# Performance work log

Measured on AMD Instinct MI355X. Metric: run time of the kernel, lower is better.

## Reference

```python
import jax, jax.numpy as jnp
import numpy as np

N, E = 50000, 800000          # nodes, directed edges
IN_DIM, HC, OUT_DIM = 128, 64, 128
NEG_SLOPE = 0.2               # PyG GATConv default leaky_relu slope
EPS = 1e-5                    # PyG LayerNorm default eps


def setup_inputs() -> dict:
    key = jax.random.key(0)
    ks = jax.random.split(key, 10)
    s = 0.1
    return {
        "x": jax.random.normal(ks[0], (N, IN_DIM), jnp.float32),
        "edge_index": jax.random.randint(ks[1], (2, E), 0, N, dtype=jnp.int32),
        # conv1: GATConv(IN_DIM -> HC, heads=2, concat=True)
        "W1": jax.random.normal(ks[2], (IN_DIM, 2 * HC), jnp.float32) * s,
        "att_src1": jax.random.normal(ks[3], (2, HC), jnp.float32) * s,
        "att_dst1": jax.random.normal(ks[4], (2, HC), jnp.float32) * s,
        "b1": jnp.zeros((2 * HC,), jnp.float32),
        "ln1_w": jnp.ones((2 * HC,), jnp.float32),
        "ln1_b": jnp.zeros((2 * HC,), jnp.float32),
        # conv2: GATConv(2*HC -> OUT_DIM, heads=1, concat=False)
        "W2": jax.random.normal(ks[5], (2 * HC, OUT_DIM), jnp.float32) * s,
        "att_src2": jax.random.normal(ks[6], (1, OUT_DIM), jnp.float32) * s,
        "att_dst2": jax.random.normal(ks[7], (1, OUT_DIM), jnp.float32) * s,
        "b2": jnp.zeros((OUT_DIM,), jnp.float32),
        "ln2_w": jnp.ones((OUT_DIM,), jnp.float32),
        "ln2_b": jnp.zeros((OUT_DIM,), jnp.float32),
    }


def gat_conv(x, src, dst, W, att_src, att_dst, bias, heads, C, concat):
    """PyG GATConv (shared lin for src/dst, self-loops already in src/dst)."""
    n = x.shape[0]
    h = (x @ W).reshape(n, heads, C)                       # [N,H,C]
    a_src = jnp.einsum('nhc,hc->nh', h, att_src)           # [N,H]
    a_dst = jnp.einsum('nhc,hc->nh', h, att_dst)           # [N,H]
    e = jax.nn.leaky_relu(a_src[src] + a_dst[dst], NEG_SLOPE)   # [E',H]
    # numerically-stable softmax over incoming edges of each dst node
    emax = jax.ops.segment_max(e, dst, num_segments=n)     # [N,H] (self-loops => non-empty)
    ex = jnp.exp(e - emax[dst])
    denom = jax.ops.segment_sum(ex, dst, num_segments=n)
    alpha = ex / (denom[dst] + 1e-16)                      # [E',H]
    out = jax.ops.segment_sum(h[src] * alpha[:, :, None], dst, num_segments=n)  # [N,H,C]
    out = out.reshape(n, heads * C) if concat else out.mean(axis=1)
    return out + bias


def graph_layernorm(x, w, b):
    """PyG LayerNorm, mode='graph', single graph: normalize over ALL nodes+features."""
    mean = x.mean()
    xc = x - mean
    var = (xc * xc).mean()
    return xc * jax.lax.rsqrt(var + EPS) * w + b


def reference(x, edge_index, W1, att_src1, att_dst1, b1, ln1_w, ln1_b,
              W2, att_src2, att_dst2, b2, ln2_w, ln2_b):
    n = x.shape[0]
    loop = jnp.arange(n, dtype=edge_index.dtype)
    src = jnp.concatenate([edge_index[0], loop])           # add self-loops for GAT convs
    dst = jnp.concatenate([edge_index[1], loop])

    h = gat_conv(x, src, dst, W1, att_src1, att_dst1, b1, heads=2, C=HC, concat=True)
    h = jax.nn.relu(graph_layernorm(h, ln1_w, ln1_b))
    h = gat_conv(h, src, dst, W2, att_src2, att_dst2, b2, heads=1, C=OUT_DIM, concat=False)
    h = graph_layernorm(h, ln2_w, ln2_b)

    # SimpleConv(aggr='mean') over the ORIGINAL edges (no self-loops), then residual
    s0, d0 = edge_index[0], edge_index[1]
    agg = jax.ops.segment_sum(h[s0], d0, num_segments=n)
    cnt = jax.ops.segment_sum(jnp.ones(s0.shape, h.dtype), d0, num_segments=n)
    mean_agg = agg / jnp.maximum(cnt, 1.0)[:, None]
    return jax.nn.relu(mean_agg + x)
```

## Files before the change

### kernel.cpp

```cpp
#include <hip/hip_runtime.h>
#include <hip/hip_bf16.h>
#include <cstdint>
#include <cstddef>

#define NN 50000
#define EE 800000
#define DD 128
#define NEG 0.2f
#define EPSL 1e-5f

#define NB   196
#define EPB  4096
#define NBKT 196
#define HM   (NBKT * NB)

#define GROWS 64

typedef __hip_bfloat16 bf16;
typedef short short8 __attribute__((ext_vector_type(8)));
typedef float f32x4 __attribute__((ext_vector_type(4)));

__device__ inline float bflo(unsigned u) { return __uint_as_float(u << 16); }
__device__ inline float bfhi(unsigned u) { return __uint_as_float(u & 0xffff0000u); }

__device__ inline unsigned short f2bf(float f) {
    __bf16 h = (__bf16)f;
    return __builtin_bit_cast(unsigned short, h);
}
__device__ inline unsigned pack2(float a, float b) {
    return (unsigned)f2bf(a) | ((unsigned)f2bf(b) << 16);
}

__device__ inline void store4(float* Out, size_t idx, float4 v) {
    *(float4*)&Out[idx] = v;
}
__device__ inline void store4(bf16* Out, size_t idx, float4 v) {
    union { bf16 b[4]; ushort4 u; } cv;
    cv.b[0] = (bf16)v.x; cv.b[1] = (bf16)v.y; cv.b[2] = (bf16)v.z; cv.b[3] = (bf16)v.w;
    *(ushort4*)&Out[idx] = cv.u;
}


__global__ __launch_bounds__(256) void hist_kernel(const int* __restrict__ ei,
                                                   int* __restrict__ histG) {
    __shared__ int lh[NBKT];
    int tid = threadIdx.x;
    for (int t = tid; t < NBKT; t += 256) lh[t] = 0;
    __syncthreads();
    int base = blockIdx.x * EPB;
    #pragma unroll
    for (int j = 0; j < EPB / 256; ++j) {
        int i = base + j * 256 + tid;
        if (i < EE) {
            unsigned d = (unsigned)ei[EE + i];
            atomicAdd(&lh[d >> 8], 1);
        }
    }
    __syncthreads();
    for (int t = tid; t < NBKT; t += 256) histG[t * NB + blockIdx.x] = lh[t];
}

__global__ __launch_bounds__(1024) void scan_hist_kernel(const int* __restrict__ histG,
                                                         int* __restrict__ offs,
                                                         int* __restrict__ bstart) {
    __shared__ int wsum[16];
    __shared__ int carry_s;
    int tid = threadIdx.x, lane = tid & 63, wv = tid >> 6;
    if (tid == 0) carry_s = 0;
    __syncthreads();
    for (int base = 0; base < HM; base += 4096) {
        int i4 = base + tid * 4;
        int4 v = make_int4(0, 0, 0, 0);
        if (i4 + 3 < HM) v = *(const int4*)&histG[i4];
        else {
            if (i4 + 0 < HM) v.x = histG[i4 + 0];
            if (i4 + 1 < HM) v.y = histG[i4 + 1];
            if (i4 + 2 < HM) v.z = histG[i4 + 2];
            if (i4 + 3 < HM) v.w = histG[i4 + 3];
        }
        int tsum = v.x + v.y + v.z + v.w;
        int x = tsum;
        for (int off = 1; off < 64; off <<= 1) {
            int t = __shfl_up(x, off);
            if (lane >= off) x += t;
        }
        if (lane == 63) wsum[wv] = x;
        __syncthreads();
        if (wv == 0) {
            int s = (lane < 16) ? wsum[lane] : 0;
            for (int off = 1; off < 16; off <<= 1) {
                int t = __shfl_up(s, off);
                if (lane >= off) s += t;
            }
            if (lane < 16) wsum[lane] = s;
        }
        __syncthreads();
        int waveoff = (wv == 0) ? 0 : wsum[wv - 1];
        int carry = carry_s;
        int o0 = carry + waveoff + x - tsum;
        int o1 = o0 + v.x, o2 = o1 + v.y, o3 = o2 + v.z;
        if (i4 + 3 < HM) *(int4*)&offs[i4] = make_int4(o0, o1, o2, o3);
        else {
            if (i4 + 0 < HM) offs[i4 + 0] = o0;
            if (i4 + 1 < HM) offs[i4 + 1] = o1;
            if (i4 + 2 < HM) offs[i4 + 2] = o2;
            if (i4 + 3 < HM) offs[i4 + 3] = o3;
        }
        if (i4 < HM && (i4 % NB) == 0) bstart[i4 / NB] = o0;
        __syncthreads();
        if (tid == 0) carry_s += wsum[15];
        __syncthreads();
    }
    if (tid == 0) bstart[NBKT] = carry_s;
}

__global__ __launch_bounds__(256) void scatter_pass1_kernel(const int* __restrict__ ei,
                                                            const int* __restrict__ offs,
                                                            unsigned* __restrict__ tmp) {
    __shared__ int lofs[NBKT];
    int tid = threadIdx.x;
    for (int t = tid; t < NBKT; t += 256) lofs[t] = offs[t * NB + blockIdx.x];
    __syncthreads();
    int base = blockIdx.x * EPB;
    #pragma unroll
    for (int j = 0; j < EPB / 256; ++j) {
        int i = base + j * 256 + tid;
        if (i < EE) {
            unsigned s = (unsigned)ei[i];
            unsigned d = (unsigned)ei[EE + i];
            unsigned key = (d << 16) | s;
            int pos = atomicAdd(&lofs[d >> 8], 1);
            tmp[pos] = key;
        }
    }
}

__global__ __launch_bounds__(256) void bucket_sort_kernel(const unsigned* __restrict__ tmp,
                                                          const int* __restrict__ bstart,
                                                          unsigned* __restrict__ col,
                                                          int* __restrict__ row_ptr) {
    __shared__ int cnt[256];
    __shared__ int cpos[256];
    __shared__ int wtot[4];
    int tid = threadIdx.x, lane = tid & 63, wv = tid >> 6;
    int s0 = bstart[blockIdx.x], s1 = bstart[blockIdx.x + 1];
    cnt[tid] = 0;
    __syncthreads();
    for (int i = s0 + tid; i < s1; i += 256)
        atomicAdd(&cnt[(tmp[i] >> 16) & 0xFF], 1);
    __syncthreads();
    int v = cnt[tid];
    int x = v;
    for (int off = 1; off < 64; off <<= 1) {
        int t = __shfl_up(x, off);
        if (lane >= off) x += t;
    }
    if (lane == 63) wtot[wv] = x;
    __syncthreads();
    int add = 0;
    for (int k = 0; k < wv; ++k) add += wtot[k];
    int start = s0 + add + x - v;
    cpos[tid] = start;
    int d = blockIdx.x * 256 + tid;
    if (d <= NN) row_ptr[d] = start;
    __syncthreads();
    for (int i = s0 + tid; i < s1; i += 256) {
        unsigned key = tmp[i];
        int pos = atomicAdd(&cpos[(key >> 16) & 0xFF], 1);
        col[pos] = key;
    }
}

template <int H, bool LN>
__global__ __launch_bounds__(512) void gemm_attn(const float* __restrict__ X,
                                                 const float* __restrict__ W,
                                                 const float* __restrict__ att_s,
                                                 const float* __restrict__ att_d,
                                                 const double* __restrict__ stats,
                                                 const float* __restrict__ lnw,
                                                 const float* __restrict__ lnb,
                                                 bf16* __restrict__ Hout,
                                                 float* __restrict__ a_src,
                                                 float* __restrict__ a_dst) {
    __shared__ __align__(16) char lds[(128 * 136 + 64 * 136) * 2 + 2048];
    unsigned short* Bt = (unsigned short*)lds;
    unsigned short* As = (unsigned short*)(lds + 128 * 136 * 2);
    float* Cs = (float*)lds;
    float* psum = (float*)(lds + (128 * 136 + 64 * 136) * 2);

    int tid = threadIdx.x;
    int row0 = blockIdx.x * GROWS;

    {
        int c = tid & 127, kg = tid >> 7;
        #pragma unroll 2
        for (int i = 0; i < 8; ++i) {
            int k0 = i * 16 + kg * 4;
            float wa = W[(size_t)(k0 + 0) * DD + c];
            float wb = W[(size_t)(k0 + 1) * DD + c];
            float wcv = W[(size_t)(k0 + 2) * DD + c];
            float wdv = W[(size_t)(k0 + 3) * DD + c];
            uint2 pk = make_uint2(pack2(wa, wb), pack2(wcv, wdv));
            *(uint2*)&Bt[c * 136 + k0] = pk;
        }
    }
    {
        int sub = tid & 31, rq = tid >> 5;
        int c4 = sub * 4;
        float mean = 0.f, inv = 1.f;
        float4 lw4 = make_float4(1.f, 1.f, 1.f, 1.f), lb4 = make_float4(0.f, 0.f, 0.f, 0.f);
        if (LN) {
            const double M = (double)NN * DD;
            double mean_d = stats[0] / M;
            double var_d = stats[1] / M - mean_d * mean_d;
            mean = (float)mean_d;
            inv = rsqrtf((float)var_d + EPSL);
            lw4 = *(const float4*)&lnw[c4];
            lb4 = *(const float4*)&lnb[c4];
        }
        #pragma unroll
        for (int i = 0; i < 4; ++i) {
            int r = i * 16 + rq;
            int row = row0 + r;
            float4 xv = make_float4(0.f, 0.f, 0.f, 0.f);
            if (row < NN) xv = *(const float4*)&X[(size_t)row * DD + c4];
            if (LN) {
                xv.x = fmaxf((xv.x - mean) * inv * lw4.x + lb4.x, 0.f);
                xv.y = fmaxf((xv.y - mean) * inv * lw4.y + lb4.y, 0.f);
                xv.z = fmaxf((xv.z - mean) * inv * lw4.z + lb4.z, 0.f);
                xv.w = fmaxf((xv.w - mean) * inv * lw4.w + lb4.w, 0.f);
            }
            uint2 pk = make_uint2(pack2(xv.x, xv.y), pack2(xv.z, xv.w));
            *(uint2*)&As[r * 136 + c4] = pk;
        }
    }
    __syncthreads();

    int lane = tid & 63, w = tid >> 6;
    int rg = w & 3, cg = w >> 2;
    int l15 = lane & 15, quad = lane >> 4;
    f32x4 acc[4];
    #pragma unroll
    for (int t = 0; t < 4; ++t) acc[t] = 0.f;
    const unsigned short* Arow = As + (rg * 16 + l15) * 136 + quad * 8;
    const unsigned short* Brow = Bt + l15 * 136 + quad * 8;
    #pragma unroll
    for (int ks = 0; ks < 4; ++ks) {
        short8 a = *(const short8*)(Arow + ks * 32);
        #pragma unroll
        for (int tt = 0; tt < 4; ++tt) {
            short8 b = *(const short8*)(Brow + (cg * 4 + tt) * 16 * 136 + ks * 32);
            acc[tt] = __builtin_amdgcn_mfma_f32_16x16x32_bf16(a, b, acc[tt], 0, 0, 0);
        }
    }
    __syncthreads();

    #pragma unroll
    for (int tt = 0; tt < 4; ++tt)
        #pragma unroll
        for (int r = 0; r < 4; ++r)
            Cs[(rg * 16 + quad * 4 + r) * 132 + (cg * 4 + tt) * 16 + l15] = acc[tt][r];

    float ds[4] = {0.f, 0.f, 0.f, 0.f}, dd[4] = {0.f, 0.f, 0.f, 0.f};
    #pragma unroll
    for (int tt = 0; tt < 4; ++tt) {
        int cc = (cg * 4 + tt) * 16 + l15;
        float as_ = att_s[cc], ad_ = att_d[cc];
        #pragma unroll
        for (int r = 0; r < 4; ++r) {
            ds[r] = fmaf(acc[tt][r], as_, ds[r]);
            dd[r] = fmaf(acc[tt][r], ad_, dd[r]);
        }
    }
    #pragma unroll
    for (int off = 1; off < 16; off <<= 1) {
        #pragma unroll
        for (int r = 0; r < 4; ++r) {
            ds[r] += __shfl_xor(ds[r], off);
            dd[r] += __shfl_xor(dd[r], off);
        }
    }
    if (l15 == 0) {
        #pragma unroll
        for (int r = 0; r < 4; ++r) {
            int rr = rg * 16 + quad * 4 + r;
            int row = row0 + rr;
            if (H == 2) {
                if (row < NN) {
                    a_src[row * 2 + cg] = ds[r];
                    a_dst[row * 2 + cg] = dd[r];
                }
            } else {
                psum[cg * 64 + rr] = ds[r];
                psum[128 + cg * 64 + rr] = dd[r];
            }
        }
    }
    __syncthreads();

    if (H == 1 && tid < 64) {
        int row = row0 + tid;
        if (row < NN) {
            a_src[row] = psum[tid] + psum[64 + tid];
            a_dst[row] = psum[128 + tid] + psum[192 + tid];
        }
    }

    {
        int sub = tid & 31, rq = tid >> 5;
        int c4 = sub * 4;
        unsigned short* Hp = (unsigned short*)Hout;
        #pragma unroll
        for (int i = 0; i < 4; ++i) {
            int r = i * 16 + rq;
            int row = row0 + r;
            if (row < NN) {
                float4 cv = *(const float4*)&Cs[r * 132 + c4];
                ushort4 pk;
                pk.x = f2bf(cv.x); pk.y = f2bf(cv.y);
                pk.z = f2bf(cv.z); pk.w = f2bf(cv.w);
                *(ushort4*)&Hp[(size_t)row * DD + c4] = pk;
            }
        }
    }
}

template <int H, typename OT>
__global__ __launch_bounds__(256) void gat_agg(const int* __restrict__ row_ptr,
                                               const unsigned* __restrict__ col,
                                               const bf16* __restrict__ Hin,
                                               const float* __restrict__ a_src,
                                               const float* __restrict__ a_dst,
                                               const float* __restrict__ bias,
                                               OT* __restrict__ Out,
                                               float2* __restrict__ pstats) {
    int tid = threadIdx.x;
    int sl = tid & 31;
    int n = blockIdx.x * 8 + (tid >> 5);
    int c0 = sl * 4;
    const int head4 = (H == 2) ? (sl >> 4) : 0;

    int beg = row_ptr[n], end = row_ptr[n + 1];
    int deg = end - beg;

    float ad0 = a_dst[n * H + 0];
    float ad1 = (H == 2) ? a_dst[n * H + 1] : 0.f;
    const ushort* Hp = (const ushort*)Hin + c0;

    float acc[4] = {0.f, 0.f, 0.f, 0.f};
    float dl0 = 0.f, dl1 = 0.f;

    for (int base = 0; base < deg; base += 32) {
        int ecnt = min(32, deg - base);
        int sv = 0; float w0v = 0.f, w1v = 0.f;
        if (sl < ecnt) {
            sv = (int)(col[beg + base + sl] & 0xffffu);
            if (H == 2) {
                float2 av = *(const float2*)&a_src[sv * 2];
                float e0 = av.x + ad0; e0 = (e0 > 0.f) ? e0 : NEG * e0;
                float e1 = av.y + ad1; e1 = (e1 > 0.f) ? e1 : NEG * e1;
                w0v = __expf(e0); w1v = __expf(e1);
                dl0 += w0v; dl1 += w1v;
            } else {
                float e0 = a_src[sv] + ad0; e0 = (e0 > 0.f) ? e0 : NEG * e0;
                w0v = __expf(e0);
                dl0 += w0v;
            }
        }
        int j = 0;
        for (; j + 7 < ecnt; j += 8) {
            int s[8]; float ww[8];
            uint2 h[8];
            #pragma unroll
            for (int u = 0; u < 8; ++u) {
                s[u] = __shfl(sv, j + u, 32);
                if (H == 2) {
                    float a0 = __shfl(w0v, j + u, 32), b0 = __shfl(w1v, j + u, 32);
                    ww[u] = head4 ? b0 : a0;
                } else {
                    ww[u] = __shfl(w0v, j + u, 32);
                }
            }
            #pragma unroll
            for (int u = 0; u < 8; ++u) h[u] = *(const uint2*)(Hp + (size_t)s[u] * DD);
            #pragma unroll
            for (int u = 0; u < 8; ++u) {
                acc[0] = fmaf(ww[u], bflo(h[u].x), acc[0]);
                acc[1] = fmaf(ww[u], bfhi(h[u].x), acc[1]);
                acc[2] = fmaf(ww[u], bflo(h[u].y), acc[2]);
                acc[3] = fmaf(ww[u], bfhi(h[u].y), acc[3]);
            }
        }
        for (; j < ecnt; ++j) {
            int s = __shfl(sv, j, 32);
            float w;
            if (H == 2) {
                float a0 = __shfl(w0v, j, 32), b0 = __shfl(w1v, j, 32);
                w = head4 ? b0 : a0;
            } else {
                w = __shfl(w0v, j, 32);
            }
            uint2 hv = *(const uint2*)(Hp + (size_t)s * DD);
            acc[0] = fmaf(w, bflo(hv.x), acc[0]); acc[1] = fmaf(w, bfhi(hv.x), acc[1]);
            acc[2] = fmaf(w, bflo(hv.y), acc[2]); acc[3] = fmaf(w, bfhi(hv.y), acc[3]);
        }
    }

    #pragma unroll
    for (int off = 1; off < 32; off <<= 1) {
        dl0 += __shfl_xor(dl0, off);
        if (H == 2) dl1 += __shfl_xor(dl1, off);
    }

    float e0 = a_src[n * H + 0] + ad0; e0 = (e0 > 0.f) ? e0 : NEG * e0;
    float ws0 = __expf(e0);
    float ws1 = 0.f;
    if (H == 2) {
        float e1 = a_src[n * H + 1] + ad1; e1 = (e1 > 0.f) ? e1 : NEG * e1;
        ws1 = __expf(e1);
    }
    float den = (H == 2 && head4) ? (dl1 + ws1) : (dl0 + ws0);
    float wself = (H == 2 && head4) ? ws1 : ws0;
    float rinv = 1.f / (den + 1e-16f);
    uint2 hs = *(const uint2*)(Hp + (size_t)n * DD);
    float4 bi = *(const float4*)&bias[c0];
    float4 o;
    o.x = fmaf(wself, bflo(hs.x), acc[0]) * rinv + bi.x;
    o.y = fmaf(wself, bfhi(hs.x), acc[1]) * rinv + bi.y;
    o.z = fmaf(wself, bflo(hs.y), acc[2]) * rinv + bi.z;
    o.w = fmaf(wself, bfhi(hs.y), acc[3]) * rinv + bi.w;
    store4(Out, (size_t)n * DD + c0, o);

    float t1 = o.x + o.y + o.z + o.w;
    float t2 = o.x * o.x + o.y * o.y + o.z * o.z + o.w * o.w;
    #pragma unroll
    for (int off = 1; off < 32; off <<= 1) {
        t1 += __shfl_xor(t1, off);
        t2 += __shfl_xor(t2, off);
    }
    if (sl == 0) pstats[n] = make_float2(t1, t2);
}

__global__ __launch_bounds__(1024) void reduce_stats_kernel(const float2* __restrict__ pstats,
                                                            double* __restrict__ stats) {
    int tid = threadIdx.x, lane = tid & 63, wv = tid >> 6;
    double s1 = 0.0, s2 = 0.0;
    for (int i = tid; i < NN; i += 1024) {
        float2 v = pstats[i];
        s1 += (double)v.x; s2 += (double)v.y;
    }
    for (int off = 32; off; off >>= 1) {
        s1 += __shfl_xor(s1, off);
        s2 += __shfl_xor(s2, off);
    }
    __shared__ double w1[16], w2[16];
    if (lane == 0) { w1[wv] = s1; w2[wv] = s2; }
    __syncthreads();
    if (tid == 0) {
        double a = 0.0, b = 0.0;
        for (int i = 0; i < 16; ++i) { a += w1[i]; b += w2[i]; }
        stats[0] = a; stats[1] = b;
    }
}

__global__ __launch_bounds__(256) void simpleconv_kernel(const int* __restrict__ row_ptr,
                                                         const unsigned* __restrict__ col,
                                                         const bf16* __restrict__ Hin,
                                                         const float* __restrict__ X,
                                                         const double* __restrict__ stats,
                                                         const float* __restrict__ lnw,
                                                         const float* __restrict__ lnb,
                                                         float* __restrict__ Out) {
    int tid = threadIdx.x;
    int sl = tid & 31;
    int n = blockIdx.x * 8 + (tid >> 5);
    int c0 = sl * 4;
    int beg = row_ptr[n], end = row_ptr[n + 1];
    int deg = end - beg;
    const ushort* Hp = (const ushort*)Hin + c0;

    float acc[4] = {0.f, 0.f, 0.f, 0.f};
    for (int base = 0; base < deg; base += 32) {
        int ecnt = min(32, deg - base);
        int sv = 0;
        if (sl < ecnt) sv = (int)(col[beg + base + sl] & 0xffffu);
        int j = 0;
        for (; j + 7 < ecnt; j += 8) {
            int s[8]; uint2 h[8];
            #pragma unroll
            for (int u = 0; u < 8; ++u) s[u] = __shfl(sv, j + u, 32);
            #pragma unroll
            for (int u = 0; u < 8; ++u) h[u] = *(const uint2*)(Hp + (size_t)s[u] * DD);
            #pragma unroll
            for (int u = 0; u < 8; ++u) {
                acc[0] += bflo(h[u].x); acc[1] += bfhi(h[u].x);
                acc[2] += bflo(h[u].y); acc[3] += bfhi(h[u].y);
            }
        }
        for (; j < ecnt; ++j) {
            int s = __shfl(sv, j, 32);
            uint2 hv = *(const uint2*)(Hp + (size_t)s * DD);
            acc[0] += bflo(hv.x); acc[1] += bfhi(hv.x);
            acc[2] += bflo(hv.y); acc[3] += bfhi(hv.y);
        }
    }

    const double M = (double)NN * DD;
    double mean_d = stats[0] / M;
    double var_d = stats[1] / M - mean_d * mean_d;
    float mean2 = (float)mean_d;
    float inv2 = rsqrtf((float)var_d + EPSL);
    float rc = 1.f / (float)((deg > 0) ? deg : 1);
    float4 xr = *(const float4*)&X[(size_t)n * DD + c0];
    float4 o;
    if (deg > 0) {
        float4 lw = *(const float4*)&lnw[c0];
        float4 lb = *(const float4*)&lnb[c0];
        o.x = (acc[0] * rc - mean2) * inv2 * lw.x + lb.x;
        o.y = (acc[1] * rc - mean2) * inv2 * lw.y + lb.y;
        o.z = (acc[2] * rc - mean2) * inv2 * lw.z + lb.z;
        o.w = (acc[3] * rc - mean2) * inv2 * lw.w + lb.w;
    } else {
        o.x = o.y = o.z = o.w = 0.f;
    }
    o.x = fmaxf(o.x + xr.x, 0.f);
    o.y = fmaxf(o.y + xr.y, 0.f);
    o.z = fmaxf(o.z + xr.z, 0.f);
    o.w = fmaxf(o.w + xr.w, 0.f);
    *(float4*)&Out[(size_t)n * DD + c0] = o;
}

extern "C" void kernel_launch(void* const* d_in, const int* in_sizes, int n_in,
                              void* d_out, int out_size, void* d_ws, size_t ws_size,
                              hipStream_t stream) {
    const float* x    = (const float*)d_in[0];
    const int*   ei   = (const int*)d_in[1];
    const float* W1   = (const float*)d_in[2];
    const float* as1  = (const float*)d_in[3];
    const float* ad1  = (const float*)d_in[4];
    const float* b1   = (const float*)d_in[5];
    const float* ln1w = (const float*)d_in[6];
    const float* ln1b = (const float*)d_in[7];
    const float* W2   = (const float*)d_in[8];
    const float* as2  = (const float*)d_in[9];
    const float* ad2  = (const float*)d_in[10];
    const float* b2   = (const float*)d_in[11];
    const float* ln2w = (const float*)d_in[12];
    const float* ln2b = (const float*)d_in[13];
    float* out = (float*)d_out;

    char* p = (char*)d_ws;
    auto alloc = [&](size_t bytes) {
        void* r = (void*)p;
        p += (bytes + 255) & ~(size_t)255;
        return r;
    };
    unsigned* tmp     = (unsigned*)alloc((size_t)EE * 4);
    unsigned* col     = (unsigned*)alloc((size_t)EE * 4);
    int*      histG   = (int*)alloc((size_t)HM * 4);
    int*      offs    = (int*)alloc((size_t)HM * 4);
    int*      bstart  = (int*)alloc((size_t)(NBKT + 1) * 4);
    int*      row_ptr = (int*)alloc((size_t)(NN + 256) * 4);
    double*   stats1  = (double*)alloc(16);
    double*   stats2  = (double*)alloc(16);
    float2*   pstats  = (float2*)alloc((size_t)NN * 8);
    bf16*     bufH    = (bf16*)alloc((size_t)NN * DD * 2);
    float*    bufF    = (float*)alloc((size_t)NN * DD * 4);
    bf16*     out2    = (bf16*)bufF;
    float*    aS1     = (float*)alloc((size_t)NN * 2 * 4);
    float*    aD1     = (float*)alloc((size_t)NN * 2 * 4);
    float*    aS2     = (float*)alloc((size_t)NN * 4);
    float*    aD2     = (float*)alloc((size_t)NN * 4);

    hist_kernel<<<NB, 256, 0, stream>>>(ei, histG);
    scan_hist_kernel<<<1, 1024, 0, stream>>>(histG, offs, bstart);
    scatter_pass1_kernel<<<NB, 256, 0, stream>>>(ei, offs, tmp);
    bucket_sort_kernel<<<NBKT, 256, 0, stream>>>(tmp, bstart, col, row_ptr);

    const int GB = (NN + GROWS - 1) / GROWS;
    const int AB = NN / 8;

    gemm_attn<2, false><<<GB, 512, 0, stream>>>(x, W1, as1, ad1,
                                                nullptr, nullptr, nullptr,
                                                bufH, aS1, aD1);
    gat_agg<2, float><<<AB, 256, 0, stream>>>(row_ptr, col, bufH, aS1, aD1, b1, bufF, pstats);
    reduce_stats_kernel<<<1, 1024, 0, stream>>>(pstats, stats1);

    gemm_attn<1, true><<<GB, 512, 0, stream>>>(bufF, W2, as2, ad2,
                                               stats1, ln1w, ln1b,
                                               bufH, aS2, aD2);
    gat_agg<1, bf16><<<AB, 256, 0, stream>>>(row_ptr, col, bufH, aS2, aD2, b2, out2, pstats);
    reduce_stats_kernel<<<1, 1024, 0, stream>>>(pstats, stats2);

    simpleconv_kernel<<<AB, 256, 0, stream>>>(row_ptr, col, out2, x,
                                              stats2, ln2w, ln2b, out);
}
```

Before: 296.1 us.

## Store layer-1 output as bf16, vectorize edge loads, reduce stats per block

The first GAT aggregation now writes its output in bf16 instead of fp32, and the second GEMM reads bf16 input through a new template parameter. This halves that intermediate's write and read traffic. The histogram and scatter kernels load edge indices as int4, four per thread. The per-node LayerNorm partial sums are combined per block in shared memory, so the final reduce reads 6250 entries instead of 50000. The bf16 intermediate adds rounding error before the LayerNorm statistics and the second layer.

```diff
diff --git a/kernel.cpp b/kernel.cpp
--- a/kernel.cpp
+++ b/kernel.cpp
@@ -15,6 +15,7 @@
 #define HM   (NBKT * NB)
 
 #define GROWS 64
+#define AB    (NN / 8)
 
 typedef __hip_bfloat16 bf16;
 typedef short short8 __attribute__((ext_vector_type(8)));
@@ -22,6 +23,7 @@
 
 __device__ inline float bflo(unsigned u) { return __uint_as_float(u << 16); }
 __device__ inline float bfhi(unsigned u) { return __uint_as_float(u & 0xffff0000u); }
+__device__ inline float bf2f(unsigned short u) { return __uint_as_float((unsigned)u << 16); }
 
 __device__ inline unsigned short f2bf(float f) {
     __bf16 h = (__bf16)f;
@@ -49,11 +51,14 @@
     __syncthreads();
     int base = blockIdx.x * EPB;
     #pragma unroll
-    for (int j = 0; j < EPB / 256; ++j) {
-        int i = base + j * 256 + tid;
-        if (i < EE) {
-            unsigned d = (unsigned)ei[EE + i];
-            atomicAdd(&lh[d >> 8], 1);
+    for (int j = 0; j < EPB / 1024; ++j) {
+        int i4 = base + (j * 256 + tid) * 4;
+        if (i4 < EE) {
+            int4 d4 = *(const int4*)&ei[EE + i4];
+            atomicAdd(&lh[(unsigned)d4.x >> 8], 1);
+            atomicAdd(&lh[(unsigned)d4.y >> 8], 1);
+            atomicAdd(&lh[(unsigned)d4.z >> 8], 1);
+            atomicAdd(&lh[(unsigned)d4.w >> 8], 1);
         }
     }
     __syncthreads();
@@ -123,14 +128,19 @@
     __syncthreads();
     int base = blockIdx.x * EPB;
     #pragma unroll
-    for (int j = 0; j < EPB / 256; ++j) {
-        int i = base + j * 256 + tid;
-        if (i < EE) {
-            unsigned s = (unsigned)ei[i];
-            unsigned d = (unsigned)ei[EE + i];
-            unsigned key = (d << 16) | s;
-            int pos = atomicAdd(&lofs[d >> 8], 1);
-            tmp[pos] = key;
+    for (int j = 0; j < EPB / 1024; ++j) {
+        int i4 = base + (j * 256 + tid) * 4;
+        if (i4 < EE) {
+            int4 s4 = *(const int4*)&ei[i4];
+            int4 d4 = *(const int4*)&ei[EE + i4];
+            unsigned k0 = ((unsigned)d4.x << 16) | (unsigned)s4.x;
+            unsigned k1 = ((unsigned)d4.y << 16) | (unsigned)s4.y;
+            unsigned k2 = ((unsigned)d4.z << 16) | (unsigned)s4.z;
+            unsigned k3 = ((unsigned)d4.w << 16) | (unsigned)s4.w;
+            tmp[atomicAdd(&lofs[(unsigned)d4.x >> 8], 1)] = k0;
+            tmp[atomicAdd(&lofs[(unsigned)d4.y >> 8], 1)] = k1;
+            tmp[atomicAdd(&lofs[(unsigned)d4.z >> 8], 1)] = k2;
+            tmp[atomicAdd(&lofs[(unsigned)d4.w >> 8], 1)] = k3;
         }
     }
 }
@@ -171,8 +181,8 @@
     }
 }
 
-template <int H, bool LN>
-__global__ __launch_bounds__(512) void gemm_attn(const float* __restrict__ X,
+template <int H, bool LN, typename XT>
+__global__ __launch_bounds__(512) void gemm_attn(const XT* __restrict__ X,
                                                  const float* __restrict__ W,
                                                  const float* __restrict__ att_s,
                                                  const float* __restrict__ att_d,
@@ -223,7 +233,14 @@
             int r = i * 16 + rq;
             int row = row0 + r;
             float4 xv = make_float4(0.f, 0.f, 0.f, 0.f);
-            if (row < NN) xv = *(const float4*)&X[(size_t)row * DD + c4];
+            if (row < NN) {
+                if constexpr (sizeof(XT) == 4) {
+                    xv = *(const float4*)&((const float*)X)[(size_t)row * DD + c4];
+                } else {
+                    ushort4 xb = *(const ushort4*)&((const unsigned short*)X)[(size_t)row * DD + c4];
+                    xv = make_float4(bf2f(xb.x), bf2f(xb.y), bf2f(xb.z), bf2f(xb.w));
+                }
+            }
             if (LN) {
                 xv.x = fmaxf((xv.x - mean) * inv * lw4.x + lb4.x, 0.f);
                 xv.y = fmaxf((xv.y - mean) * inv * lw4.y + lb4.y, 0.f);
@@ -336,7 +353,8 @@
                                                float2* __restrict__ pstats) {
     int tid = threadIdx.x;
     int sl = tid & 31;
-    int n = blockIdx.x * 8 + (tid >> 5);
+    int hw = tid >> 5;
+    int n = blockIdx.x * 8 + hw;
     int c0 = sl * 4;
     const int head4 = (H == 2) ? (sl >> 4) : 0;
 
@@ -438,14 +456,22 @@
         t1 += __shfl_xor(t1, off);
         t2 += __shfl_xor(t2, off);
     }
-    if (sl == 0) pstats[n] = make_float2(t1, t2);
+    __shared__ float2 ps[8];
+    if (sl == 0) ps[hw] = make_float2(t1, t2);
+    __syncthreads();
+    if (tid == 0) {
+        float a = 0.f, b = 0.f;
+        #pragma unroll
+        for (int k = 0; k < 8; ++k) { a += ps[k].x; b += ps[k].y; }
+        pstats[blockIdx.x] = make_float2(a, b);
+    }
 }
 
 __global__ __launch_bounds__(1024) void reduce_stats_kernel(const float2* __restrict__ pstats,
                                                             double* __restrict__ stats) {
     int tid = threadIdx.x, lane = tid & 63, wv = tid >> 6;
     double s1 = 0.0, s2 = 0.0;
-    for (int i = tid; i < NN; i += 1024) {
+    for (int i = tid; i < AB; i += 1024) {
         float2 v = pstats[i];
         s1 += (double)v.x; s2 += (double)v.y;
     }
@@ -563,10 +589,9 @@
     int*      row_ptr = (int*)alloc((size_t)(NN + 256) * 4);
     double*   stats1  = (double*)alloc(16);
     double*   stats2  = (double*)alloc(16);
-    float2*   pstats  = (float2*)alloc((size_t)NN * 8);
-    bf16*     bufH    = (bf16*)alloc((size_t)NN * DD * 2);
-    float*    bufF    = (float*)alloc((size_t)NN * DD * 4);
-    bf16*     out2    = (bf16*)bufF;
+    float2*   pstats  = (float2*)alloc((size_t)AB * 8);
+    bf16*     bufA    = (bf16*)alloc((size_t)NN * DD * 2);
+    bf16*     bufB    = (bf16*)alloc((size_t)NN * DD * 2);
     float*    aS1     = (float*)alloc((size_t)NN * 2 * 4);
     float*    aD1     = (float*)alloc((size_t)NN * 2 * 4);
     float*    aS2     = (float*)alloc((size_t)NN * 4);
@@ -578,20 +603,19 @@
     bucket_sort_kernel<<<NBKT, 256, 0, stream>>>(tmp, bstart, col, row_ptr);
 
     const int GB = (NN + GROWS - 1) / GROWS;
-    const int AB = NN / 8;
-
-    gemm_attn<2, false><<<GB, 512, 0, stream>>>(x, W1, as1, ad1,
-                                                nullptr, nullptr, nullptr,
-                                                bufH, aS1, aD1);
-    gat_agg<2, float><<<AB, 256, 0, stream>>>(row_ptr, col, bufH, aS1, aD1, b1, bufF, pstats);
+
+    gemm_attn<2, false, float><<<GB, 512, 0, stream>>>(x, W1, as1, ad1,
+                                                       nullptr, nullptr, nullptr,
+                                                       bufA, aS1, aD1);
+    gat_agg<2, bf16><<<AB, 256, 0, stream>>>(row_ptr, col, bufA, aS1, aD1, b1, bufB, pstats);
     reduce_stats_kernel<<<1, 1024, 0, stream>>>(pstats, stats1);
 
-    gemm_attn<1, true><<<GB, 512, 0, stream>>>(bufF, W2, as2, ad2,
-                                               stats1, ln1w, ln1b,
-                                               bufH, aS2, aD2);
-    gat_agg<1, bf16><<<AB, 256, 0, stream>>>(row_ptr, col, bufH, aS2, aD2, b2, out2, pstats);
+    gemm_attn<1, true, bf16><<<GB, 512, 0, stream>>>(bufB, W2, as2, ad2,
+                                                     stats1, ln1w, ln1b,
+                                                     bufA, aS2, aD2);
+    gat_agg<1, bf16><<<AB, 256, 0, stream>>>(row_ptr, col, bufA, aS2, aD2, b2, bufB, pstats);
     reduce_stats_kernel<<<1, 1024, 0, stream>>>(pstats, stats2);
 
-    simpleconv_kernel<<<AB, 256, 0, stream>>>(row_ptr, col, out2, x,
+    simpleconv_kernel<<<AB, 256, 0, stream>>>(row_ptr, col, bufB, x,
                                               stats2, ln2w, ln2b, out);
 }
```

Measured after the change: 274.7 us. 7.2% less time.
